# Optimization experiments

Hardware: AMD Instinct MI355X
Metric: run time of the kernel (lower is better)

The kernel has to match this reference:

```python
import jax, jax.numpy as jnp
import numpy as np

N_NODES = 50000
N_EDGES = 800000
F_IN = 128
HID = 128
N_CLASSES = 2
N_GRAPHS = 500
NEG_SLOPE = 0.2


def setup_inputs() -> dict:
    key = jax.random.key(0)
    ks = jax.random.split(key, 16)
    inp = {
        "x": jax.random.normal(ks[0], (N_NODES, F_IN), dtype=jnp.float32),
        "edge_index": jax.random.randint(ks[1], (2, N_EDGES), 0, N_NODES, dtype=jnp.int64),
        "batch": jnp.sort(jax.random.randint(ks[2], (N_NODES,), 0, N_GRAPHS, dtype=jnp.int64)),
    }
    dims = [(F_IN, HID), (HID, HID), (HID, HID)]
    for i, (din, dout) in enumerate(dims, start=1):
        s = 1.0 / np.sqrt(din)
        inp[f"W{i}"] = jax.random.uniform(ks[3 * i], (din, dout), minval=-s, maxval=s, dtype=jnp.float32)
        inp[f"a_src{i}"] = jax.random.uniform(ks[3 * i + 1], (dout,), minval=-s, maxval=s, dtype=jnp.float32)
        inp[f"a_dst{i}"] = jax.random.uniform(ks[3 * i + 2], (dout,), minval=-s, maxval=s, dtype=jnp.float32)
        inp[f"b{i}"] = jnp.zeros((dout,), dtype=jnp.float32)
    s = 1.0 / np.sqrt(HID)
    inp["W_lin"] = jax.random.uniform(ks[12], (HID, N_CLASSES), minval=-s, maxval=s, dtype=jnp.float32)
    inp["b_lin"] = jax.random.uniform(ks[13], (N_CLASSES,), minval=-s, maxval=s, dtype=jnp.float32)
    return inp


def gat_conv(x, src, dst, W, a_src, a_dst, b, n_nodes):
    # single-head PyG GATConv (heads=1, concat), self-loops already in src/dst
    h = x @ W                                   # [N, dout]
    alpha_src = h @ a_src                       # [N]
    alpha_dst = h @ a_dst                       # [N]
    e = jax.nn.leaky_relu(alpha_src[src] + alpha_dst[dst], NEG_SLOPE)  # [E]
    # segment softmax over edges grouped by destination node
    m = jax.ops.segment_max(e, dst, num_segments=n_nodes)
    ex = jnp.exp(e - m[dst])
    denom = jax.ops.segment_sum(ex, dst, num_segments=n_nodes)
    alpha = ex / denom[dst]                     # [E]
    out = jax.ops.segment_sum(h[src] * alpha[:, None], dst, num_segments=n_nodes)
    return out + b


def reference(x, edge_index, batch, W1, a_src1, a_dst1, b1, W2, a_src2, a_dst2, b2,
              W3, a_src3, a_dst3, b3, W_lin, b_lin):
    n = x.shape[0]
    loops = jnp.arange(n, dtype=edge_index.dtype)
    src = jnp.concatenate([edge_index[0], loops])
    dst = jnp.concatenate([edge_index[1], loops])

    h = jax.nn.relu(gat_conv(x, src, dst, W1, a_src1, a_dst1, b1, n))
    h = jax.nn.relu(gat_conv(h, src, dst, W2, a_src2, a_dst2, b2, n))
    h = gat_conv(h, src, dst, W3, a_src3, a_dst3, b3, n)

    # global mean pool over graphs
    sums = jax.ops.segment_sum(h, batch, num_segments=N_GRAPHS)       # [G, HID]
    counts = jax.ops.segment_sum(jnp.ones((n,), h.dtype), batch, num_segments=N_GRAPHS)
    pooled = sums / jnp.maximum(counts, 1.0)[:, None]
    # dropout is identity in eval mode
    return pooled @ W_lin + b_lin
```

## Files before the change

kernel.cpp:

```cpp
#include <hip/hip_runtime.h>
#include <math.h>

#define N_NODES  50000
#define N_EDGES  800000
#define FDIM     128
#define N_GRAPHS 500
#define NEG_SLOPE 0.2f
#define EN_TOTAL (N_EDGES + N_NODES)
#define GEMM_TILES (N_NODES / 16)
#define WT_COLS 144
#define PREP_PLANE_BLOCKS 1024
#define BSHIFT 8
#define BWIDTH 256
#define NBUCK ((N_NODES + BWIDTH - 1) / BWIDTH)
#define BIN_BATCH 8192
#define BIN_BLOCKS ((EN_TOTAL + BIN_BATCH - 1) / BIN_BATCH)
#define PREP_GRID (3 + PREP_PLANE_BLOCKS + BIN_BLOCKS)

typedef short bf16x8 __attribute__((ext_vector_type(8)));
typedef float f32x4 __attribute__((ext_vector_type(4)));

static __device__ __forceinline__ float lrelu(float x) {
    return x >= 0.f ? x : NEG_SLOPE * x;
}
static __device__ __forceinline__ unsigned short f2bf(float v) {
    unsigned int u = __float_as_uint(v);
    u += 0x7fffu + ((u >> 16) & 1u);
    return (unsigned short)(u >> 16);
}
static __device__ __forceinline__ float bf2f(unsigned short s) {
    return __uint_as_float(((unsigned int)s) << 16);
}

__global__ __launch_bounds__(256) void prep_all(
    const float* __restrict__ X, const int* __restrict__ ei,
    const float* __restrict__ W0, const float* __restrict__ W1,
    const float* __restrict__ W2,
    const float* __restrict__ as0, const float* __restrict__ as1,
    const float* __restrict__ as2,
    const float* __restrict__ ad0, const float* __restrict__ ad1,
    const float* __restrict__ ad2,
    unsigned short* __restrict__ WT,
    unsigned short* __restrict__ PHI, unsigned short* __restrict__ PLO,
    int* __restrict__ bcnt_part)
{
    __shared__ float wa[256];
    __shared__ int hist[BWIDTH];
    const int b = blockIdx.x, tid = threadIdx.x;

    if (b < 3) {
        const float* W  = (b == 0) ? W0  : (b == 1) ? W1  : W2;
        const float* As = (b == 0) ? as0 : (b == 1) ? as1 : as2;
        const float* Ad = (b == 0) ? ad0 : (b == 1) ? ad1 : ad2;
        unsigned short* hi = WT + (size_t)b * 2 * WT_COLS * FDIM;
        unsigned short* lo = hi + WT_COLS * FDIM;
        {
            const int k = tid & 127;
            const float* av = (tid < 128) ? As : Ad;
            float s = 0.f;
            for (int c = 0; c < 128; ++c) s += W[k * FDIM + c] * av[c];
            wa[tid] = s;
        }
        __syncthreads();
        for (int i = tid; i < FDIM * FDIM; i += 256) {
            const int k = i >> 7, c = i & 127;
            const float v = W[i];
            const unsigned short h = f2bf(v);
            hi[c * FDIM + k] = h;
            lo[c * FDIM + k] = f2bf(v - bf2f(h));
        }
        for (int k = tid; k < FDIM; k += 256) {
            const float vs = wa[k], vd = wa[128 + k];
            const unsigned short hs = f2bf(vs), hd = f2bf(vd);
            hi[128 * FDIM + k] = hs; lo[128 * FDIM + k] = f2bf(vs - bf2f(hs));
            hi[129 * FDIM + k] = hd; lo[129 * FDIM + k] = f2bf(vd - bf2f(hd));
        }
        for (int i = tid; i < 14 * FDIM; i += 256) {
            hi[130 * FDIM + i] = 0;
            lo[130 * FDIM + i] = 0;
        }
    } else if (b < 3 + PREP_PLANE_BLOCKS) {
        const int total = N_NODES * FDIM / 4;
        for (int i = (b - 3) * 256 + tid; i < total; i += PREP_PLANE_BLOCKS * 256) {
            const float4 v = ((const float4*)X)[i];
            ushort4 h4, l4;
            h4.x = f2bf(v.x); l4.x = f2bf(v.x - bf2f(h4.x));
            h4.y = f2bf(v.y); l4.y = f2bf(v.y - bf2f(h4.y));
            h4.z = f2bf(v.z); l4.z = f2bf(v.z - bf2f(h4.z));
            h4.w = f2bf(v.w); l4.w = f2bf(v.w - bf2f(h4.w));
            ((ushort4*)PHI)[i] = h4;
            ((ushort4*)PLO)[i] = l4;
        }
    } else {
        const int cb = b - 3 - PREP_PLANE_BLOCKS;
        if (tid < BWIDTH) hist[tid] = 0;
        __syncthreads();
        const int i0 = cb * BIN_BATCH;
        const int i1 = min(i0 + BIN_BATCH, EN_TOTAL);
        for (int i = i0 + tid; i < i1; i += 256) {
            const int d = (i < N_EDGES) ? ei[N_EDGES + i] : (i - N_EDGES);
            atomicAdd(&hist[d >> BSHIFT], 1);
        }
        __syncthreads();
        if (tid < BWIDTH) bcnt_part[cb * BWIDTH + tid] = hist[tid];
    }
}

__global__ __launch_bounds__(256) void gemm_mfma8(
    const unsigned short* __restrict__ PHI, const unsigned short* __restrict__ PLO,
    const unsigned short* __restrict__ WThi, const unsigned short* __restrict__ WTlo,
    unsigned short* __restrict__ Hb, float* __restrict__ asrcN, float* __restrict__ adstN)
{
    __shared__ unsigned short sH[16 * 128];
    __shared__ unsigned short sL[16 * 128];

    const int tid = threadIdx.x, wv = tid >> 6, lane = tid & 63;
    const int r16 = lane & 15, g = lane >> 4;
    const int t0 = wv * 2;
    const int tile = blockIdx.x;

    {
        const int srow = wv * 4 + (lane >> 4);
        const int sslot = lane & 15;
        const int ldsOfs = srow * 128 + ((sslot ^ (srow & 7)) * 8);
        const size_t go = (size_t)tile * 16 * FDIM + (size_t)srow * FDIM + sslot * 8;
        *(uint4*)(&sH[ldsOfs]) = *(const uint4*)(PHI + go);
        *(uint4*)(&sL[ldsOfs]) = *(const uint4*)(PLO + go);
    }

    bf16x8 bh[2][4], bl[2][4];
    #pragma unroll
    for (int tt = 0; tt < 2; ++tt) {
        const int c = (t0 + tt) * 16 + r16;
        #pragma unroll
        for (int cc = 0; cc < 4; ++cc) {
            bh[tt][cc] = *(const bf16x8*)(WThi + c * FDIM + cc * 32 + 8 * g);
            bl[tt][cc] = *(const bf16x8*)(WTlo + c * FDIM + cc * 32 + 8 * g);
        }
    }
    __syncthreads();

    bf16x8 ah[4], al[4];
    #pragma unroll
    for (int cc = 0; cc < 4; ++cc) {
        const int p = (cc * 4 + g) ^ (r16 & 7);
        const int ofs = r16 * 128 + p * 8;
        ah[cc] = *(const bf16x8*)(&sH[ofs]);
        al[cc] = *(const bf16x8*)(&sL[ofs]);
    }

    f32x4 acc0 = {0.f, 0.f, 0.f, 0.f}, acc1 = {0.f, 0.f, 0.f, 0.f};
    #pragma unroll
    for (int cc = 0; cc < 4; ++cc) {
        acc0 = __builtin_amdgcn_mfma_f32_16x16x32_bf16(ah[cc], bh[0][cc], acc0, 0, 0, 0);
        acc1 = __builtin_amdgcn_mfma_f32_16x16x32_bf16(ah[cc], bh[1][cc], acc1, 0, 0, 0);
        acc0 = __builtin_amdgcn_mfma_f32_16x16x32_bf16(al[cc], bh[0][cc], acc0, 0, 0, 0);
        acc1 = __builtin_amdgcn_mfma_f32_16x16x32_bf16(al[cc], bh[1][cc], acc1, 0, 0, 0);
        acc0 = __builtin_amdgcn_mfma_f32_16x16x32_bf16(ah[cc], bl[0][cc], acc0, 0, 0, 0);
        acc1 = __builtin_amdgcn_mfma_f32_16x16x32_bf16(ah[cc], bl[1][cc], acc1, 0, 0, 0);
    }

    const int m0 = tile * 16;
    const int rowb = m0 + 4 * g;
    #pragma unroll
    for (int r = 0; r < 4; ++r) {
        Hb[(size_t)(rowb + r) * FDIM + (t0 + 0) * 16 + r16] = f2bf(acc0[r]);
        Hb[(size_t)(rowb + r) * FDIM + (t0 + 1) * 16 + r16] = f2bf(acc1[r]);
    }

    if (wv == (tile & 3)) {
        const unsigned short* WThiE = WThi + (128 + r16) * FDIM + 8 * g;
        const unsigned short* WTloE = WTlo + (128 + r16) * FDIM + 8 * g;
        f32x4 acce = {0.f, 0.f, 0.f, 0.f};
        #pragma unroll
        for (int cc = 0; cc < 4; ++cc) {
            const bf16x8 bhe = *(const bf16x8*)(WThiE + cc * 32);
            const bf16x8 ble = *(const bf16x8*)(WTloE + cc * 32);
            acce = __builtin_amdgcn_mfma_f32_16x16x32_bf16(ah[cc], bhe, acce, 0, 0, 0);
            acce = __builtin_amdgcn_mfma_f32_16x16x32_bf16(al[cc], bhe, acce, 0, 0, 0);
            acce = __builtin_amdgcn_mfma_f32_16x16x32_bf16(ah[cc], ble, acce, 0, 0, 0);
        }
        if (r16 == 0) {
            #pragma unroll
            for (int r = 0; r < 4; ++r) asrcN[rowb + r] = acce[r];
        } else if (r16 == 1) {
            #pragma unroll
            for (int r = 0; r < 4; ++r) adstN[rowb + r] = acce[r];
        }
    }
}

__global__ __launch_bounds__(256) void bucket_scan(const int* __restrict__ bcnt_part,
                                                   int* __restrict__ bbase,
                                                   int* __restrict__ bcur,
                                                   int* __restrict__ off) {
    __shared__ int s[256];
    const int tid = threadIdx.x;
    int sum = 0;
    for (int p = 0; p < BIN_BLOCKS; ++p) sum += bcnt_part[p * BWIDTH + tid];
    s[tid] = (tid < NBUCK) ? sum : 0;
    __syncthreads();
    #pragma unroll
    for (int d = 1; d < 256; d <<= 1) {
        int t = (tid >= d) ? s[tid - d] : 0;
        __syncthreads();
        s[tid] += t;
        __syncthreads();
    }
    if (tid < NBUCK) {
        const int base = (tid == 0) ? 0 : s[tid - 1];
        bbase[tid] = base;
        bcur[tid] = base;
    }
    if (tid == 0) { bbase[NBUCK] = EN_TOTAL; off[N_NODES] = EN_TOTAL; }
}

__global__ __launch_bounds__(256) void bin_edges(const int* __restrict__ ei,
                                                 const int* __restrict__ bcnt_part,
                                                 int* __restrict__ bcur,
                                                 unsigned int* __restrict__ ebuf) {
    __shared__ int hist[NBUCK], base[NBUCK];
    const int tid = threadIdx.x;
    if (tid < NBUCK) {
        const int h = bcnt_part[blockIdx.x * BWIDTH + tid];
        base[tid] = h ? atomicAdd(&bcur[tid], h) : 0;
        hist[tid] = 0;
    }
    __syncthreads();
    const int i0 = blockIdx.x * BIN_BATCH;
    const int i1 = min(i0 + BIN_BATCH, EN_TOTAL);
    for (int i = i0 + tid; i < i1; i += 256) {
        int s, d;
        if (i < N_EDGES) { s = ei[i]; d = ei[N_EDGES + i]; }
        else             { s = d = i - N_EDGES; }
        const int b = d >> BSHIFT;
        const int r = atomicAdd(&hist[b], 1);
        ebuf[base[b] + r] = ((unsigned int)(d & (BWIDTH - 1)) << 17) | (unsigned int)s;
    }
}

__global__ __launch_bounds__(512) void place_edges(
    const int* __restrict__ bbase, const unsigned int* __restrict__ ebuf,
    int* __restrict__ off, int* __restrict__ srcs)
{
    __shared__ int hist[BWIDTH], scn[BWIDTH];
    const int b = blockIdx.x, tid = threadIdx.x;
    const int d0 = b << BSHIFT;
    const int nd = min(BWIDTH, N_NODES - d0);
    const int bstart = bbase[b], bend = bbase[b + 1];

    if (tid < BWIDTH) hist[tid] = 0;
    __syncthreads();
    for (int i = bstart + tid; i < bend; i += 512)
        atomicAdd(&hist[ebuf[i] >> 17], 1);
    __syncthreads();
    if (tid < BWIDTH) scn[tid] = hist[tid];
    __syncthreads();
    #pragma unroll
    for (int d = 1; d < BWIDTH; d <<= 1) {
        int t = (tid < BWIDTH && tid >= d) ? scn[tid - d] : 0;
        __syncthreads();
        if (tid < BWIDTH) scn[tid] += t;
        __syncthreads();
    }
    if (tid < nd) {
        const int start = bstart + (tid ? scn[tid - 1] : 0);
        off[d0 + tid] = start;
        hist[tid] = start;
    }
    __syncthreads();
    for (int i = bstart + tid; i < bend; i += 512) {
        const unsigned int e = ebuf[i];
        const int p = atomicAdd(&hist[e >> 17], 1);
        srcs[p] = (int)(e & 0x1FFFFu);
    }
}

__global__ __launch_bounds__(256) void gat_aggregate(
    const unsigned short* __restrict__ Hb, const int* __restrict__ off,
    const int* __restrict__ srcs,
    const float* __restrict__ asrcN, const float* __restrict__ adstN,
    const float* __restrict__ bias,
    unsigned short* __restrict__ PHI, unsigned short* __restrict__ PLO,
    float* __restrict__ OUTF, int mode)
{
    const int wave = threadIdx.x >> 6, lane = threadIdx.x & 63;
    const int grp = lane >> 3, fl = lane & 7;

    for (int n = blockIdx.x * 4 + wave; n < N_NODES; n += gridDim.x * 4) {
        const int s0 = off[n], s1 = off[n + 1];
        const int deg = s1 - s0;
        const float ad = adstN[n];

        float e_reg = -1e30f;
        float m = -1e30f;
        for (int j = s0 + lane; j < s1; j += 64) {
            float e = lrelu(asrcN[srcs[j]] + ad);
            if (j - s0 < 64) e_reg = e;
            m = fmaxf(m, e);
        }
        #pragma unroll
        for (int o = 32; o; o >>= 1) m = fmaxf(m, __shfl_xor(m, o));
        const float ex_reg = (lane < deg) ? __expf(e_reg - m) : 0.f;

        float4 a0 = {0,0,0,0}, a1 = {0,0,0,0}, a2 = {0,0,0,0}, a3 = {0,0,0,0};
        float dn = 0.f;
        const unsigned short* Hf = Hb + (size_t)fl * 16;
        for (int j = s0 + grp; j < s1; j += 8) {
            const int s = srcs[j];
            const float ex = (deg <= 64)
                ? __shfl(ex_reg, j - s0)
                : __expf(lrelu(asrcN[s] + ad) - m);
            dn += ex;
            const uint4* hp = (const uint4*)(Hf + (size_t)s * FDIM);
            const uint4 u0 = hp[0], u1 = hp[1];
            a0.x += ex * __uint_as_float(u0.x << 16);
            a0.y += ex * __uint_as_float(u0.x & 0xffff0000u);
            a0.z += ex * __uint_as_float(u0.y << 16);
            a0.w += ex * __uint_as_float(u0.y & 0xffff0000u);
            a1.x += ex * __uint_as_float(u0.z << 16);
            a1.y += ex * __uint_as_float(u0.z & 0xffff0000u);
            a1.z += ex * __uint_as_float(u0.w << 16);
            a1.w += ex * __uint_as_float(u0.w & 0xffff0000u);
            a2.x += ex * __uint_as_float(u1.x << 16);
            a2.y += ex * __uint_as_float(u1.x & 0xffff0000u);
            a2.z += ex * __uint_as_float(u1.y << 16);
            a2.w += ex * __uint_as_float(u1.y & 0xffff0000u);
            a3.x += ex * __uint_as_float(u1.z << 16);
            a3.y += ex * __uint_as_float(u1.z & 0xffff0000u);
            a3.z += ex * __uint_as_float(u1.w << 16);
            a3.w += ex * __uint_as_float(u1.w & 0xffff0000u);
        }

        #pragma unroll
        for (int o = 8; o <= 32; o <<= 1) {
            dn  += __shfl_xor(dn, o);
            a0.x += __shfl_xor(a0.x, o); a0.y += __shfl_xor(a0.y, o);
            a0.z += __shfl_xor(a0.z, o); a0.w += __shfl_xor(a0.w, o);
            a1.x += __shfl_xor(a1.x, o); a1.y += __shfl_xor(a1.y, o);
            a1.z += __shfl_xor(a1.z, o); a1.w += __shfl_xor(a1.w, o);
            a2.x += __shfl_xor(a2.x, o); a2.y += __shfl_xor(a2.y, o);
            a2.z += __shfl_xor(a2.z, o); a2.w += __shfl_xor(a2.w, o);
            a3.x += __shfl_xor(a3.x, o); a3.y += __shfl_xor(a3.y, o);
            a3.z += __shfl_xor(a3.z, o); a3.w += __shfl_xor(a3.w, o);
        }

        if (grp == 0) {
            const float rd = 1.f / dn;
            const float4* bp = (const float4*)(bias + fl * 16);
            float4 ov[4] = {a0, a1, a2, a3};
            #pragma unroll
            for (int q = 0; q < 4; ++q) {
                const float4 b4 = bp[q];
                float4 o4;
                o4.x = ov[q].x * rd + b4.x; o4.y = ov[q].y * rd + b4.y;
                o4.z = ov[q].z * rd + b4.z; o4.w = ov[q].w * rd + b4.w;
                if (mode == 0) {
                    o4.x = fmaxf(o4.x, 0.f); o4.y = fmaxf(o4.y, 0.f);
                    o4.z = fmaxf(o4.z, 0.f); o4.w = fmaxf(o4.w, 0.f);
                    ushort4 h4, l4;
                    h4.x = f2bf(o4.x); l4.x = f2bf(o4.x - bf2f(h4.x));
                    h4.y = f2bf(o4.y); l4.y = f2bf(o4.y - bf2f(h4.y));
                    h4.z = f2bf(o4.z); l4.z = f2bf(o4.z - bf2f(h4.z));
                    h4.w = f2bf(o4.w); l4.w = f2bf(o4.w - bf2f(h4.w));
                    const size_t base = (size_t)n * FDIM + fl * 16 + q * 4;
                    *(ushort4*)(PHI + base) = h4;
                    *(ushort4*)(PLO + base) = l4;
                } else {
                    *(float4*)(OUTF + (size_t)n * FDIM + fl * 16 + q * 4) = o4;
                }
            }
        }
    }
}

__global__ __launch_bounds__(256) void pool_linear2(
    const float* __restrict__ H, const int* __restrict__ batch,
    const float* __restrict__ Wlin, const float* __restrict__ blin,
    float* __restrict__ out)
{
    const int g = blockIdx.x, tid = threadIdx.x;
    const int rl = tid >> 5, fq = tid & 31;

    int a = 0, b = N_NODES;
    while (a < b) { int mid = (a + b) >> 1; if (batch[mid] < g) a = mid + 1; else b = mid; }
    const int lo = a;
    b = N_NODES;
    while (a < b) { int mid = (a + b) >> 1; if (batch[mid] <= g) a = mid + 1; else b = mid; }
    const int hi = a;

    float4 acc = {0.f, 0.f, 0.f, 0.f};
    for (int n = lo + rl; n < hi; n += 8) {
        const float4 v = *(const float4*)(H + (size_t)n * FDIM + fq * 4);
        acc.x += v.x; acc.y += v.y; acc.z += v.z; acc.w += v.w;
    }
    __shared__ float4 s[8][32];
    s[rl][fq] = acc;
    __syncthreads();

    if (tid < 32) {
        float4 t = s[0][fq];
        #pragma unroll
        for (int r = 1; r < 8; ++r) {
            const float4 v = s[r][fq];
            t.x += v.x; t.y += v.y; t.z += v.z; t.w += v.w;
        }
        const float inv = 1.f / fmaxf((float)(hi - lo), 1.f);
        t.x *= inv; t.y *= inv; t.z *= inv; t.w *= inv;
        float d0 = t.x * Wlin[(fq * 4 + 0) * 2 + 0] + t.y * Wlin[(fq * 4 + 1) * 2 + 0]
                 + t.z * Wlin[(fq * 4 + 2) * 2 + 0] + t.w * Wlin[(fq * 4 + 3) * 2 + 0];
        float d1 = t.x * Wlin[(fq * 4 + 0) * 2 + 1] + t.y * Wlin[(fq * 4 + 1) * 2 + 1]
                 + t.z * Wlin[(fq * 4 + 2) * 2 + 1] + t.w * Wlin[(fq * 4 + 3) * 2 + 1];
        #pragma unroll
        for (int o = 1; o <= 16; o <<= 1) {
            d0 += __shfl_xor(d0, o);
            d1 += __shfl_xor(d1, o);
        }
        if (fq == 0) {
            out[g * 2 + 0] = d0 + blin[0];
            out[g * 2 + 1] = d1 + blin[1];
        }
    }
}

extern "C" void kernel_launch(void* const* d_in, const int* in_sizes, int n_in,
                              void* d_out, int out_size, void* d_ws, size_t ws_size,
                              hipStream_t stream)
{
    const float* x     = (const float*)d_in[0];
    const int*   ei    = (const int*)d_in[1];
    const int*   batch = (const int*)d_in[2];
    const float* W[3]    = {(const float*)d_in[3],  (const float*)d_in[7],  (const float*)d_in[11]};
    const float* avs[3]  = {(const float*)d_in[4],  (const float*)d_in[8],  (const float*)d_in[12]};
    const float* avd[3]  = {(const float*)d_in[5],  (const float*)d_in[9],  (const float*)d_in[13]};
    const float* bias[3] = {(const float*)d_in[6],  (const float*)d_in[10], (const float*)d_in[14]};
    const float* Wlin = (const float*)d_in[15];
    const float* blin = (const float*)d_in[16];
    float* out = (float*)d_out;

    char* w = (char*)d_ws;
    unsigned short* PHI = (unsigned short*)w; w += (size_t)N_NODES * FDIM * 2;
    unsigned short* PLO = (unsigned short*)w; w += (size_t)N_NODES * FDIM * 2;
    float* hOf = (float*)PHI;
    unsigned short* Hb = (unsigned short*)w; w += (size_t)N_NODES * FDIM * 2;
    float* attn  = (float*)w; w += 2 * 200192;
    int*   off   = (int*)w;   w += 200192;
    int*   bcnt_part = (int*)w; w += (size_t)BIN_BLOCKS * BWIDTH * 4;
    int*   bbase = (int*)w;   w += 1024;
    int*   bcur  = (int*)w;   w += 1024;
    int*   srcs  = (int*)w;   w += (size_t)EN_TOTAL * 4;
    unsigned int* ebuf = (unsigned int*)w; w += (size_t)EN_TOTAL * 4;
    unsigned short* WT = (unsigned short*)w; w += (size_t)3 * 2 * WT_COLS * FDIM * 2;
    float* asrcN = attn;
    float* adstN = attn + N_NODES;

    prep_all<<<PREP_GRID, 256, 0, stream>>>(x, ei, W[0], W[1], W[2],
                                            avs[0], avs[1], avs[2],
                                            avd[0], avd[1], avd[2],
                                            WT, PHI, PLO, bcnt_part);

    bucket_scan<<<1, 256, 0, stream>>>(bcnt_part, bbase, bcur, off);
    bin_edges<<<BIN_BLOCKS, 256, 0, stream>>>(ei, bcnt_part, bcur, ebuf);
    place_edges<<<NBUCK, 512, 0, stream>>>(bbase, ebuf, off, srcs);

    for (int l = 0; l < 3; ++l) {
        const unsigned short* WThi = WT + (size_t)l * 2 * WT_COLS * FDIM;
        const unsigned short* WTlo = WThi + WT_COLS * FDIM;
        gemm_mfma8<<<GEMM_TILES, 256, 0, stream>>>(PHI, PLO, WThi, WTlo, Hb, asrcN, adstN);
        gat_aggregate<<<2048, 256, 0, stream>>>(Hb, off, srcs, asrcN, adstN, bias[l],
                                                PHI, PLO, hOf, (l < 2) ? 0 : 1);
    }

    pool_linear2<<<N_GRAPHS, 256, 0, stream>>>(hOf, batch, Wlin, blin, out);
}
```

Before: 316.9 us.

## Make feature GEMM persistent with double-buffered direct-to-LDS tile prefetch

New measurement: 288.7 us. 1.1x faster.

```diff
diff --git a/kernel.cpp b/kernel.cpp
--- a/kernel.cpp
+++ b/kernel.cpp
@@ -19,6 +19,8 @@
 
 typedef short bf16x8 __attribute__((ext_vector_type(8)));
 typedef float f32x4 __attribute__((ext_vector_type(4)));
+typedef const __attribute__((address_space(1))) void* gas_ptr;
+typedef __attribute__((address_space(3))) void* las_ptr;
 
 static __device__ __forceinline__ float lrelu(float x) {
     return x >= 0.f ? x : NEG_SLOPE * x;
@@ -106,27 +108,17 @@
     }
 }
 
-__global__ __launch_bounds__(256) void gemm_mfma8(
+__global__ __launch_bounds__(256) void gemm_mfma9(
     const unsigned short* __restrict__ PHI, const unsigned short* __restrict__ PLO,
     const unsigned short* __restrict__ WThi, const unsigned short* __restrict__ WTlo,
     unsigned short* __restrict__ Hb, float* __restrict__ asrcN, float* __restrict__ adstN)
 {
-    __shared__ unsigned short sH[16 * 128];
-    __shared__ unsigned short sL[16 * 128];
+    __shared__ unsigned short sH[2][16 * 128];
+    __shared__ unsigned short sL[2][16 * 128];
 
     const int tid = threadIdx.x, wv = tid >> 6, lane = tid & 63;
     const int r16 = lane & 15, g = lane >> 4;
     const int t0 = wv * 2;
-    const int tile = blockIdx.x;
-
-    {
-        const int srow = wv * 4 + (lane >> 4);
-        const int sslot = lane & 15;
-        const int ldsOfs = srow * 128 + ((sslot ^ (srow & 7)) * 8);
-        const size_t go = (size_t)tile * 16 * FDIM + (size_t)srow * FDIM + sslot * 8;
-        *(uint4*)(&sH[ldsOfs]) = *(const uint4*)(PHI + go);
-        *(uint4*)(&sL[ldsOfs]) = *(const uint4*)(PLO + go);
-    }
 
     bf16x8 bh[2][4], bl[2][4];
     #pragma unroll
@@ -138,55 +130,81 @@
             bl[tt][cc] = *(const bf16x8*)(WTlo + c * FDIM + cc * 32 + 8 * g);
         }
     }
-    __syncthreads();
-
-    bf16x8 ah[4], al[4];
-    #pragma unroll
-    for (int cc = 0; cc < 4; ++cc) {
-        const int p = (cc * 4 + g) ^ (r16 & 7);
-        const int ofs = r16 * 128 + p * 8;
-        ah[cc] = *(const bf16x8*)(&sH[ofs]);
-        al[cc] = *(const bf16x8*)(&sL[ofs]);
-    }
-
-    f32x4 acc0 = {0.f, 0.f, 0.f, 0.f}, acc1 = {0.f, 0.f, 0.f, 0.f};
-    #pragma unroll
-    for (int cc = 0; cc < 4; ++cc) {
-        acc0 = __builtin_amdgcn_mfma_f32_16x16x32_bf16(ah[cc], bh[0][cc], acc0, 0, 0, 0);
-        acc1 = __builtin_amdgcn_mfma_f32_16x16x32_bf16(ah[cc], bh[1][cc], acc1, 0, 0, 0);
-        acc0 = __builtin_amdgcn_mfma_f32_16x16x32_bf16(al[cc], bh[0][cc], acc0, 0, 0, 0);
-        acc1 = __builtin_amdgcn_mfma_f32_16x16x32_bf16(al[cc], bh[1][cc], acc1, 0, 0, 0);
-        acc0 = __builtin_amdgcn_mfma_f32_16x16x32_bf16(ah[cc], bl[0][cc], acc0, 0, 0, 0);
-        acc1 = __builtin_amdgcn_mfma_f32_16x16x32_bf16(ah[cc], bl[1][cc], acc1, 0, 0, 0);
-    }
-
-    const int m0 = tile * 16;
-    const int rowb = m0 + 4 * g;
-    #pragma unroll
-    for (int r = 0; r < 4; ++r) {
-        Hb[(size_t)(rowb + r) * FDIM + (t0 + 0) * 16 + r16] = f2bf(acc0[r]);
-        Hb[(size_t)(rowb + r) * FDIM + (t0 + 1) * 16 + r16] = f2bf(acc1[r]);
-    }
-
-    if (wv == (tile & 3)) {
-        const unsigned short* WThiE = WThi + (128 + r16) * FDIM + 8 * g;
-        const unsigned short* WTloE = WTlo + (128 + r16) * FDIM + 8 * g;
-        f32x4 acce = {0.f, 0.f, 0.f, 0.f};
+    const unsigned short* WThiE = WThi + (128 + r16) * FDIM + 8 * g;
+    const unsigned short* WTloE = WTlo + (128 + r16) * FDIM + 8 * g;
+
+    const int srow = wv * 4 + (lane >> 4);
+    const int gslot = (lane & 15) ^ (srow & 7);
+    const size_t gOfs0 = (size_t)srow * FDIM + gslot * 8;
+
+    int tile = blockIdx.x;
+    {
+        const size_t go = (size_t)tile * 16 * FDIM + gOfs0;
+        __builtin_amdgcn_global_load_lds((gas_ptr)(PHI + go), (las_ptr)&sH[0][wv * 512], 16, 0, 0);
+        __builtin_amdgcn_global_load_lds((gas_ptr)(PLO + go), (las_ptr)&sL[0][wv * 512], 16, 0, 0);
+    }
+    __syncthreads();
+
+    int cur = 0, rot = 0;
+    for (; tile < GEMM_TILES; tile += gridDim.x, ++rot) {
+        const int nxt = tile + (int)gridDim.x;
+        if (nxt < GEMM_TILES) {
+            const size_t go = (size_t)nxt * 16 * FDIM + gOfs0;
+            __builtin_amdgcn_global_load_lds((gas_ptr)(PHI + go),
+                                             (las_ptr)&sH[cur ^ 1][wv * 512], 16, 0, 0);
+            __builtin_amdgcn_global_load_lds((gas_ptr)(PLO + go),
+                                             (las_ptr)&sL[cur ^ 1][wv * 512], 16, 0, 0);
+        }
+
+        bf16x8 ah[4], al[4];
         #pragma unroll
         for (int cc = 0; cc < 4; ++cc) {
-            const bf16x8 bhe = *(const bf16x8*)(WThiE + cc * 32);
-            const bf16x8 ble = *(const bf16x8*)(WTloE + cc * 32);
-            acce = __builtin_amdgcn_mfma_f32_16x16x32_bf16(ah[cc], bhe, acce, 0, 0, 0);
-            acce = __builtin_amdgcn_mfma_f32_16x16x32_bf16(al[cc], bhe, acce, 0, 0, 0);
-            acce = __builtin_amdgcn_mfma_f32_16x16x32_bf16(ah[cc], ble, acce, 0, 0, 0);
-        }
-        if (r16 == 0) {
+            const int p = (cc * 4 + g) ^ (r16 & 7);
+            const int ofs = r16 * 128 + p * 8;
+            ah[cc] = *(const bf16x8*)(&sH[cur][ofs]);
+            al[cc] = *(const bf16x8*)(&sL[cur][ofs]);
+        }
+
+        f32x4 acc0 = {0.f, 0.f, 0.f, 0.f}, acc1 = {0.f, 0.f, 0.f, 0.f};
+        #pragma unroll
+        for (int cc = 0; cc < 4; ++cc) {
+            acc0 = __builtin_amdgcn_mfma_f32_16x16x32_bf16(ah[cc], bh[0][cc], acc0, 0, 0, 0);
+            acc1 = __builtin_amdgcn_mfma_f32_16x16x32_bf16(ah[cc], bh[1][cc], acc1, 0, 0, 0);
+            acc0 = __builtin_amdgcn_mfma_f32_16x16x32_bf16(al[cc], bh[0][cc], acc0, 0, 0, 0);
+            acc1 = __builtin_amdgcn_mfma_f32_16x16x32_bf16(al[cc], bh[1][cc], acc1, 0, 0, 0);
+            acc0 = __builtin_amdgcn_mfma_f32_16x16x32_bf16(ah[cc], bl[0][cc], acc0, 0, 0, 0);
+            acc1 = __builtin_amdgcn_mfma_f32_16x16x32_bf16(ah[cc], bl[1][cc], acc1, 0, 0, 0);
+        }
+
+        const int m0 = tile * 16;
+        const int rowb = m0 + 4 * g;
+        #pragma unroll
+        for (int r = 0; r < 4; ++r) {
+            Hb[(size_t)(rowb + r) * FDIM + (t0 + 0) * 16 + r16] = f2bf(acc0[r]);
+            Hb[(size_t)(rowb + r) * FDIM + (t0 + 1) * 16 + r16] = f2bf(acc1[r]);
+        }
+
+        if (wv == ((tile + rot) & 3)) {
+            f32x4 acce = {0.f, 0.f, 0.f, 0.f};
             #pragma unroll
-            for (int r = 0; r < 4; ++r) asrcN[rowb + r] = acce[r];
-        } else if (r16 == 1) {
-            #pragma unroll
-            for (int r = 0; r < 4; ++r) adstN[rowb + r] = acce[r];
-        }
+            for (int cc = 0; cc < 4; ++cc) {
+                const bf16x8 bhe = *(const bf16x8*)(WThiE + cc * 32);
+                const bf16x8 ble = *(const bf16x8*)(WTloE + cc * 32);
+                acce = __builtin_amdgcn_mfma_f32_16x16x32_bf16(ah[cc], bhe, acce, 0, 0, 0);
+                acce = __builtin_amdgcn_mfma_f32_16x16x32_bf16(al[cc], bhe, acce, 0, 0, 0);
+                acce = __builtin_amdgcn_mfma_f32_16x16x32_bf16(ah[cc], ble, acce, 0, 0, 0);
+            }
+            if (r16 == 0) {
+                #pragma unroll
+                for (int r = 0; r < 4; ++r) asrcN[rowb + r] = acce[r];
+            } else if (r16 == 1) {
+                #pragma unroll
+                for (int r = 0; r < 4; ++r) adstN[rowb + r] = acce[r];
+            }
+        }
+
+        __syncthreads();
+        cur ^= 1;
     }
 }
 
@@ -466,7 +484,7 @@
     for (int l = 0; l < 3; ++l) {
         const unsigned short* WThi = WT + (size_t)l * 2 * WT_COLS * FDIM;
         const unsigned short* WTlo = WThi + WT_COLS * FDIM;
-        gemm_mfma8<<<GEMM_TILES, 256, 0, stream>>>(PHI, PLO, WThi, WTlo, Hb, asrcN, adstN);
+        gemm_mfma9<<<1024, 256, 0, stream>>>(PHI, PLO, WThi, WTlo, Hb, asrcN, adstN);
         gat_aggregate<<<2048, 256, 0, stream>>>(Hb, off, srcs, asrcN, adstN, bias[l],
                                                 PHI, PLO, hOf, (l < 2) ? 0 : 1);
     }
```
